# Performance work log

Hardware: AMD Instinct MI355X
Metric: run time of the kernel (lower is better)

The kernel has to match this reference:

```python
import jax, jax.numpy as jnp
import numpy as np
import math

B, S, H = 8, 4096, 1024
E, I, K = 8, 2048, 2
CAP_FACTOR = 1.0


def setup_inputs() -> dict:
    key = jax.random.key(0)
    k1, k2, k3, k4 = jax.random.split(key, 4)
    # kaiming_uniform (linear): bound = sqrt(3 / fan_in), fan_in = last dim
    def kaiming(k, shape):
        bound = math.sqrt(3.0 / shape[-1])
        return jax.random.uniform(k, shape, jnp.float32, -bound, bound)
    x = jax.random.normal(k1, (B, S, H), jnp.float32)
    expert_embeddings = kaiming(k2, (E, H))
    first_linear = kaiming(k3, (E, I, H))
    second_linear = kaiming(k4, (E, H, I))
    return {"x": x, "expert_embeddings": expert_embeddings,
            "first_linear": first_linear, "second_linear": second_linear}


def _router(x, expert_embeddings):
    # dot: [B, S, E]
    dot = jnp.einsum('bsh,eh->bse', x, expert_embeddings)
    n = dot.shape[0] * dot.shape[1]
    dot2 = dot.reshape(n, E)
    vals, idx = jax.lax.top_k(dot2, K)                       # [N, K]
    rows = jnp.arange(n)[:, None]
    masked = jnp.full_like(dot2, -jnp.inf).at[rows, idx].set(vals)
    return jax.nn.softmax(masked, axis=-1)                   # [N, E]


def reference(x, expert_embeddings, first_linear, second_linear):
    batch, seq, hidden = x.shape
    n_tokens = batch * seq
    expert_capacity = math.ceil(n_tokens / E * CAP_FACTOR)

    weights = _router(x, expert_embeddings)                  # [N, E]
    ones = (weights > 0).astype(weights.dtype)               # tokens routed to expert
    # capacity mask: keep first expert_capacity tokens (in token order) per expert
    cap_ones = jnp.where(jnp.cumsum(ones, axis=0) <= expert_capacity, ones, 0.0)
    caw = weights * cap_ones                                 # [N, E]

    # topk over token dim per expert -> selected token slots
    vals, idx = jax.lax.top_k(caw.T, expert_capacity)        # [E, C]
    index = idx.reshape(-1)                                  # [E*C]

    x_flat = x.reshape(n_tokens, hidden)
    tokens = x_flat[index].reshape(E, expert_capacity, hidden)   # gather

    inter = jax.nn.relu(jnp.einsum('ech,eih->eci', tokens, first_linear))
    out = jnp.einsum('eci,ehi->ech', inter, second_linear)
    out = out * vals[:, :, None]                             # weight by router prob

    final = jnp.zeros((n_tokens, hidden), x.dtype).at[index].add(
        out.reshape(-1, hidden))                             # scatter-add combine
    return final.reshape(x.shape)
```

## Files before the change

### kernel.cpp

```cpp
#include <hip/hip_runtime.h>
#include <stdint.h>

#define N_TOK 32768
#define HID   1024
#define NE    8
#define NI    2048
#define CAP   4096

typedef short s16x8 __attribute__((ext_vector_type(8)));
typedef float f32x4 __attribute__((ext_vector_type(4)));

__device__ __forceinline__ unsigned short f2bf(float f) {
    unsigned int u = __builtin_bit_cast(unsigned int, f);
    u += 0x7fffu + ((u >> 16) & 1u);
    return (unsigned short)(u >> 16);
}

__device__ __forceinline__ void gload16(const void* g, void* l) {
    __builtin_amdgcn_global_load_lds(
        (const __attribute__((address_space(1))) unsigned int*)(uintptr_t)g,
        (__attribute__((address_space(3))) unsigned int*)(unsigned int)(uintptr_t)l,
        16, 0, 0);
}

#define WAIT_LGKM0 asm volatile("s_waitcnt lgkmcnt(0)" ::: "memory")
#define WAIT_VM6   asm volatile("s_waitcnt vmcnt(6)" ::: "memory")
#define WAIT_VM0   asm volatile("s_waitcnt vmcnt(0)" ::: "memory")
#define SFENCE     __builtin_amdgcn_sched_barrier(0)
#define BARR       __builtin_amdgcn_s_barrier()

#define STAGE(Ms, rM, tile, h) do { \
    unsigned short* _d = Ms + (((tile) & 1) * 16384) + (h) * 8192 + wave * 1024; \
    gload16(rM[h][0] + (tile) * 64 + gsl8, _d); \
    gload16(rM[h][1] + (tile) * 64 + gsl8, _d + 512); } while (0)

#define MFMA16(AF, BF, NP) do { \
    __builtin_amdgcn_s_setprio(1); \
    _Pragma("unroll") \
    for (int mi = 0; mi < 8; ++mi) { \
        acc[mi][(NP)*2]   = __builtin_amdgcn_mfma_f32_16x16x32_bf16(AF[mi], BF[(NP)*2],   acc[mi][(NP)*2],   0, 0, 0); \
        acc[mi][(NP)*2+1] = __builtin_amdgcn_mfma_f32_16x16x32_bf16(AF[mi], BF[(NP)*2+1], acc[mi][(NP)*2+1], 0, 0, 0); \
    } \
    __builtin_amdgcn_s_setprio(0); \
} while (0)

__global__ __launch_bounds__(256) void cvt_kernel(
    const float* __restrict__ src, unsigned short* __restrict__ dst, size_t n8)
{
    size_t i = (size_t)blockIdx.x * 256 + threadIdx.x;
    size_t stride = (size_t)gridDim.x * 256;
    for (; i < n8; i += stride) {
        float4 a0 = ((const float4*)src)[2 * i];
        float4 a1 = ((const float4*)src)[2 * i + 1];
        uint4 p;
        p.x = f2bf(a0.x) | ((unsigned)f2bf(a0.y) << 16);
        p.y = f2bf(a0.z) | ((unsigned)f2bf(a0.w) << 16);
        p.z = f2bf(a1.x) | ((unsigned)f2bf(a1.y) << 16);
        p.w = f2bf(a1.z) | ((unsigned)f2bf(a1.w) << 16);
        ((uint4*)dst)[i] = p;
    }
}

__global__ __launch_bounds__(256) void router_kernel(
    const float* __restrict__ x, const float* __restrict__ emb,
    int2* __restrict__ r_e, float2* __restrict__ r_w,
    unsigned short* __restrict__ xb)
{
    int token = blockIdx.x * 4 + (threadIdx.x >> 6);
    int lane  = threadIdx.x & 63;
    const float4* xr = (const float4*)(x + (size_t)token * HID);
    const float4* er = (const float4*)emb;

    float a[NE];
#pragma unroll
    for (int e = 0; e < NE; ++e) a[e] = 0.f;
    uint2 pk[4];
#pragma unroll
    for (int j = 0; j < 4; ++j) {
        float4 v = xr[j * 64 + lane];
        pk[j].x = f2bf(v.x) | ((unsigned)f2bf(v.y) << 16);
        pk[j].y = f2bf(v.z) | ((unsigned)f2bf(v.w) << 16);
#pragma unroll
        for (int e = 0; e < NE; ++e) {
            float4 w = er[e * 256 + j * 64 + lane];
            a[e] += v.x * w.x + v.y * w.y + v.z * w.z + v.w * w.w;
        }
    }
    uint2* xbr = (uint2*)(xb + (size_t)token * HID);
#pragma unroll
    for (int j = 0; j < 4; ++j) xbr[j * 64 + lane] = pk[j];

#pragma unroll
    for (int e = 0; e < NE; ++e) {
        for (int off = 32; off; off >>= 1) a[e] += __shfl_xor(a[e], off);
    }
    if (lane == 0) {
        float v1 = -1e30f, v2 = -1e30f; int i1 = 0, i2 = 0;
#pragma unroll
        for (int e = 0; e < NE; ++e) {
            float v = a[e];
            if (v > v1) { v2 = v1; i2 = i1; v1 = v; i1 = e; }
            else if (v > v2) { v2 = v; i2 = e; }
        }
        float ex = __expf(v2 - v1);
        r_e[token] = make_int2(i1, i2);
        r_w[token] = make_float2(1.f / (1.f + ex), ex / (1.f + ex));
    }
}

__global__ __launch_bounds__(1024) void count_kernel(
    const int2* __restrict__ r_e, int* __restrict__ bc)
{
    __shared__ int cnt[NE];
    if (threadIdx.x < NE) cnt[threadIdx.x] = 0;
    __syncthreads();
    int n = blockIdx.x * 1024 + threadIdx.x;
    int2 e = r_e[n];
    atomicAdd(&cnt[e.x], 1);
    atomicAdd(&cnt[e.y], 1);
    __syncthreads();
    if (threadIdx.x < NE) bc[blockIdx.x * NE + threadIdx.x] = cnt[threadIdx.x];
}

__global__ void prefix_kernel(const int* __restrict__ bc, int* __restrict__ bb)
{
    int e = threadIdx.x;
    if (e >= NE) return;
    int run = 0;
    for (int b = 0; b < N_TOK / 1024; ++b) {
        bb[b * NE + e] = run;
        run += bc[b * NE + e];
    }
}

__global__ __launch_bounds__(1024) void assign_kernel(
    const int2* __restrict__ r_e, const float2* __restrict__ r_w,
    const int* __restrict__ bb,
    int* __restrict__ tok_list, float* __restrict__ w_list)
{
    __shared__ int wavecnt[16][NE];
    __shared__ int waveoff[16][NE];
    int tid = threadIdx.x, lane = tid & 63, wv = tid >> 6;
    int n = blockIdx.x * 1024 + tid;
    int2 e = r_e[n];
    float2 w = r_w[n];
    unsigned long long below = (1ull << lane) - 1ull;
    int rank0 = 0, rank1 = 0;
#pragma unroll
    for (int ex = 0; ex < NE; ++ex) {
        unsigned long long m = __ballot(e.x == ex || e.y == ex);
        if (lane == 0) wavecnt[wv][ex] = __popcll(m);
        int r = __popcll(m & below);
        if (e.x == ex) rank0 = r;
        if (e.y == ex) rank1 = r;
    }
    __syncthreads();
    if (tid < NE) {
        int run = 0;
        for (int w2 = 0; w2 < 16; ++w2) { waveoff[w2][tid] = run; run += wavecnt[w2][tid]; }
    }
    __syncthreads();
    int s0 = bb[blockIdx.x * NE + e.x] + waveoff[wv][e.x] + rank0;
    int s1 = bb[blockIdx.x * NE + e.y] + waveoff[wv][e.y] + rank1;
    if (s0 < CAP) { tok_list[e.x * CAP + s0] = n; w_list[e.x * CAP + s0] = w.x; }
    if (s1 < CAP) { tok_list[e.y * CAP + s1] = n; w_list[e.y * CAP + s1] = w.y; }
}

__global__ __launch_bounds__(512, 2) void gemm1_k(
    const unsigned short* __restrict__ xb,
    const unsigned short* __restrict__ w1b,
    const int* __restrict__ tok_list,
    unsigned short* __restrict__ inter,
    int eb)
{
    constexpr int K = HID, T = K / 64, NTN = NI / 256;
    __shared__ __align__(16) unsigned short smem[65536];
    unsigned short* As = smem;
    unsigned short* Bs = smem + 32768;

    const int nblk = gridDim.x;
    const int lin  = blockIdx.x;
    const int wg   = (lin & 7) * (nblk >> 3) + (lin >> 3);
    const int tn = wg % NTN;
    const int tm = (wg / NTN) & 15;
    const int ez = wg / (NTN * 16);
    const int e  = eb + ez;

    const int tid = threadIdx.x, lane = tid & 63, wave = tid >> 6;
    const int wr = wave >> 2, wc = wave & 3;
    const int gsl8 = ((lane & 7) ^ (lane >> 3)) * 8;
    const int aoff = (wr * 128 + (lane & 15)) * 64;
    const int boff = (wc * 64 + (lane & 15)) * 64;
    const int ph0 = ((lane >> 4) ^ (lane & 7)) * 8;
    const int ph1 = ((4 + (lane >> 4)) ^ (lane & 7)) * 8;
    const int rbase = wave * 16 + (lane >> 3);

    const int* tl = tok_list + e * CAP + tm * 256;
    const unsigned short* rA[2][2];
    const unsigned short* rB[2][2];
#pragma unroll
    for (int h = 0; h < 2; ++h)
#pragma unroll
        for (int j = 0; j < 2; ++j) {
            rA[h][j] = xb + (size_t)tl[h * 128 + rbase + j * 8] * K;
            rB[h][j] = w1b + ((size_t)e * NI + tn * 256 + h * 128 + rbase + j * 8) * K;
        }

    f32x4 acc[8][4];
#pragma unroll
    for (int i = 0; i < 8; ++i)
#pragma unroll
        for (int j = 0; j < 4; ++j) acc[i][j] = (f32x4)0.f;

    s16x8 afr[8], bfr0[4], bfr1[4];

    STAGE(As, rA, 0, 0); STAGE(As, rA, 0, 1);
    STAGE(Bs, rB, 0, 0); STAGE(Bs, rB, 0, 1);
    STAGE(Bs, rB, 1, 0); STAGE(Bs, rB, 1, 1);
    STAGE(As, rA, 1, 0);
    WAIT_VM6; SFENCE; BARR; SFENCE;

#pragma unroll 2
    for (int t = 0; t < T; ++t) {
        const int buf = (t & 1) * 16384;
        if (t + 1 < T) STAGE(As, rA, t + 1, 1);
#pragma unroll
        for (int mi = 0; mi < 8; ++mi)
            afr[mi] = *(const s16x8*)(As + buf + aoff + mi * 1024 + ph0);
#pragma unroll
        for (int ni = 0; ni < 4; ++ni) {
            bfr0[ni] = *(const s16x8*)(Bs + buf + boff + ni * 1024 + ph0);
            bfr1[ni] = *(const s16x8*)(Bs + buf + boff + ni * 1024 + ph1);
        }
        WAIT_LGKM0; SFENCE; BARR; SFENCE;
        MFMA16(afr, bfr0, 0);
        if (t + 2 < T) STAGE(Bs, rB, t + 2, 0);
        BARR; SFENCE;
        MFMA16(afr, bfr0, 1);
        if (t + 2 < T) STAGE(Bs, rB, t + 2, 1);
#pragma unroll
        for (int mi = 0; mi < 8; ++mi)
            afr[mi] = *(const s16x8*)(As + buf + aoff + mi * 1024 + ph1);
        WAIT_LGKM0; SFENCE; BARR; SFENCE;
        MFMA16(afr, bfr1, 0);
        if (t + 2 < T) STAGE(As, rA, t + 2, 0);
        if (t < T - 2) { WAIT_VM6; } else { WAIT_VM0; }
        SFENCE; BARR; SFENCE;
        MFMA16(afr, bfr1, 1);
    }

#pragma unroll
    for (int mi = 0; mi < 8; ++mi)
#pragma unroll
        for (int ni = 0; ni < 4; ++ni)
#pragma unroll
            for (int r = 0; r < 4; ++r) {
                int row = wr * 128 + mi * 16 + (lane >> 4) * 4 + r;
                int c   = wc * 64 + ni * 16 + (lane & 15);
                float v = acc[mi][ni][r];
                v = v > 0.f ? v : 0.f;
                smem[row * 256 + (((c >> 3) ^ (row & 7)) << 3) + (c & 7)] = f2bf(v);
            }
    __syncthreads();
    unsigned short* Cp = inter + ((size_t)ez * CAP + tm * 256) * NI + tn * 256;
#pragma unroll
    for (int it = 0; it < 16; ++it) {
        int v = tid + it * 512;
        int row = v >> 5, s = v & 31;
        uint4 val = *(const uint4*)&smem[row * 256 + ((s ^ (row & 7)) << 3)];
        *(uint4*)&Cp[(size_t)row * NI + s * 8] = val;
    }
}

__global__ __launch_bounds__(512, 2) void gemm2_k(
    const unsigned short* __restrict__ inter,
    const unsigned short* __restrict__ w2b,
    const int* __restrict__ tok_list,
    const float* __restrict__ w_list,
    float* __restrict__ out,
    int eb)
{
    constexpr int K = NI, T = K / 64, NTN = HID / 256;
    __shared__ __align__(16) unsigned short smem[65536];
    unsigned short* As = smem;
    unsigned short* Bs = smem + 32768;

    const int nblk = gridDim.x;
    const int lin  = blockIdx.x;
    const int wg   = (lin & 7) * (nblk >> 3) + (lin >> 3);
    const int tn = wg % NTN;
    const int tm = (wg / NTN) & 15;
    const int ez = wg / (NTN * 16);
    const int e  = eb + ez;

    const int tid = threadIdx.x, lane = tid & 63, wave = tid >> 6;
    const int wr = wave >> 2, wc = wave & 3;
    const int gsl8 = ((lane & 7) ^ (lane >> 3)) * 8;
    const int aoff = (wr * 128 + (lane & 15)) * 64;
    const int boff = (wc * 64 + (lane & 15)) * 64;
    const int ph0 = ((lane >> 4) ^ (lane & 7)) * 8;
    const int ph1 = ((4 + (lane >> 4)) ^ (lane & 7)) * 8;
    const int rbase = wave * 16 + (lane >> 3);

    const unsigned short* rA[2][2];
    const unsigned short* rB[2][2];
#pragma unroll
    for (int h = 0; h < 2; ++h)
#pragma unroll
        for (int j = 0; j < 2; ++j) {
            rA[h][j] = inter + ((size_t)ez * CAP + tm * 256 + h * 128 + rbase + j * 8) * (size_t)K;
            rB[h][j] = w2b + ((size_t)e * HID + tn * 256 + h * 128 + rbase + j * 8) * (size_t)K;
        }

    f32x4 acc[8][4];
#pragma unroll
    for (int i = 0; i < 8; ++i)
#pragma unroll
        for (int j = 0; j < 4; ++j) acc[i][j] = (f32x4)0.f;

    s16x8 afr[8], bfr0[4], bfr1[4];

    STAGE(As, rA, 0, 0); STAGE(As, rA, 0, 1);
    STAGE(Bs, rB, 0, 0); STAGE(Bs, rB, 0, 1);
    STAGE(Bs, rB, 1, 0); STAGE(Bs, rB, 1, 1);
    STAGE(As, rA, 1, 0);
    WAIT_VM6; SFENCE; BARR; SFENCE;

#pragma unroll 2
    for (int t = 0; t < T; ++t) {
        const int buf = (t & 1) * 16384;
        if (t + 1 < T) STAGE(As, rA, t + 1, 1);
#pragma unroll
        for (int mi = 0; mi < 8; ++mi)
            afr[mi] = *(const s16x8*)(As + buf + aoff + mi * 1024 + ph0);
#pragma unroll
        for (int ni = 0; ni < 4; ++ni) {
            bfr0[ni] = *(const s16x8*)(Bs + buf + boff + ni * 1024 + ph0);
            bfr1[ni] = *(const s16x8*)(Bs + buf + boff + ni * 1024 + ph1);
        }
        WAIT_LGKM0; SFENCE; BARR; SFENCE;
        MFMA16(afr, bfr0, 0);
        if (t + 2 < T) STAGE(Bs, rB, t + 2, 0);
        BARR; SFENCE;
        MFMA16(afr, bfr0, 1);
        if (t + 2 < T) STAGE(Bs, rB, t + 2, 1);
#pragma unroll
        for (int mi = 0; mi < 8; ++mi)
            afr[mi] = *(const s16x8*)(As + buf + aoff + mi * 1024 + ph1);
        WAIT_LGKM0; SFENCE; BARR; SFENCE;
        MFMA16(afr, bfr1, 0);
        if (t + 2 < T) STAGE(As, rA, t + 2, 0);
        if (t < T - 2) { WAIT_VM6; } else { WAIT_VM0; }
        SFENCE; BARR; SFENCE;
        MFMA16(afr, bfr1, 1);
    }

    const int* tl   = tok_list + e * CAP + tm * 256;
    const float* wl = w_list  + e * CAP + tm * 256;
#pragma unroll
    for (int mi = 0; mi < 8; ++mi)
#pragma unroll
        for (int r = 0; r < 4; ++r) {
            int rrow = wr * 128 + mi * 16 + (lane >> 4) * 4 + r;
            int tok  = tl[rrow];
            float w  = wl[rrow];
            float* orow = out + (size_t)tok * HID + tn * 256 + wc * 64;
#pragma unroll
            for (int ni = 0; ni < 4; ++ni)
                atomicAdd(&orow[ni * 16 + (lane & 15)], acc[mi][ni][r] * w);
        }
}

extern "C" void kernel_launch(void* const* d_in, const int* in_sizes, int n_in,
                              void* d_out, int out_size, void* d_ws, size_t ws_size,
                              hipStream_t stream)
{
    const float* x   = (const float*)d_in[0];
    const float* emb = (const float*)d_in[1];
    const float* W1  = (const float*)d_in[2];
    const float* W2  = (const float*)d_in[3];
    float* out = (float*)d_out;

    size_t off = 0;
    auto alloc = [&](size_t bytes) -> void* {
        void* p = (char*)d_ws + off;
        off += (bytes + 255) & ~(size_t)255;
        return p;
    };
    const size_t sz_w  = (size_t)NE * NI * HID * 2;
    const size_t sz_xb = (size_t)N_TOK * HID * 2;

    int*   tok_list = (int*)alloc((size_t)NE * CAP * 4);
    float* w_list   = (float*)alloc((size_t)NE * CAP * 4);
    unsigned short* w1b = (unsigned short*)alloc(sz_w);
    unsigned short* w2b = (unsigned short*)alloc(sz_w);
    unsigned short* xb  = (unsigned short*)alloc(sz_xb);

    unsigned short* inter = (unsigned short*)((char*)d_ws + off);
    size_t avail = ws_size > off ? ws_size - off : 0;
    const size_t per_e = (size_t)CAP * NI * 2;
    int G = (avail >= 8 * per_e) ? 8 : (avail >= 4 * per_e) ? 4
          : (avail >= 2 * per_e) ? 2 : 1;

    int2*   r_e = (int2*)inter;
    float2* r_w = (float2*)((char*)inter + (size_t)N_TOK * 8);
    int*    bc  = (int*)((char*)inter + (size_t)N_TOK * 16);
    int*    bb  = bc + (N_TOK / 1024) * NE;

    hipMemsetAsync(d_out, 0, (size_t)N_TOK * HID * 4, stream);
    hipMemsetAsync(tok_list, 0, (size_t)NE * CAP * 4, stream);
    hipMemsetAsync(w_list, 0, (size_t)NE * CAP * 4, stream);

    cvt_kernel<<<2048, 256, 0, stream>>>(W1, w1b, (size_t)NE * NI * HID / 8);
    cvt_kernel<<<2048, 256, 0, stream>>>(W2, w2b, (size_t)NE * HID * NI / 8);
    router_kernel<<<N_TOK / 4, 256, 0, stream>>>(x, emb, r_e, r_w, xb);
    count_kernel<<<N_TOK / 1024, 1024, 0, stream>>>(r_e, bc);
    prefix_kernel<<<1, 64, 0, stream>>>(bc, bb);
    assign_kernel<<<N_TOK / 1024, 1024, 0, stream>>>(r_e, r_w, bb, tok_list, w_list);

    for (int eb = 0; eb < NE; eb += G) {
        gemm1_k<<<dim3((NI / 256) * 16 * G), 512, 0, stream>>>(xb, w1b, tok_list, inter, eb);
        gemm2_k<<<dim3((HID / 256) * 16 * G), 512, 0, stream>>>(inter, w2b, tok_list, w_list, out, eb);
    }
}
```

Before: 471.4 us.

## Reshape GEMM wave tiling to 4x2 and interleave LDS reads with MFMA clusters

Changes the per-wave tile in both expert GEMMs from 128x64 to 64x128 (4x2 wave grid), splitting fragment loads into A/B halves. LDS reads are now interleaved with 4x4 MFMA clusters, and all next-tile global stages are issued in one group, cutting one barrier per k-step. This aims to overlap LDS latency with MFMA work and reduce synchronization. A __syncthreads is added before the epilogue because the LDS staging buffer is reused there.

After: 472.9 us. No clear change (+0.3%).

```diff
diff --git a/kernel.cpp b/kernel.cpp
--- a/kernel.cpp
+++ b/kernel.cpp
@@ -34,14 +34,27 @@
     gload16(rM[h][0] + (tile) * 64 + gsl8, _d); \
     gload16(rM[h][1] + (tile) * 64 + gsl8, _d + 512); } while (0)
 
-#define MFMA16(AF, BF, NP) do { \
+#define MFMA_CL(AF, BF, NB) do { \
     __builtin_amdgcn_s_setprio(1); \
     _Pragma("unroll") \
-    for (int mi = 0; mi < 8; ++mi) { \
-        acc[mi][(NP)*2]   = __builtin_amdgcn_mfma_f32_16x16x32_bf16(AF[mi], BF[(NP)*2],   acc[mi][(NP)*2],   0, 0, 0); \
-        acc[mi][(NP)*2+1] = __builtin_amdgcn_mfma_f32_16x16x32_bf16(AF[mi], BF[(NP)*2+1], acc[mi][(NP)*2+1], 0, 0, 0); \
-    } \
+    for (int mi = 0; mi < 4; ++mi) \
+    _Pragma("unroll") \
+    for (int nj = 0; nj < 4; ++nj) \
+        acc[mi][(NB) + nj] = __builtin_amdgcn_mfma_f32_16x16x32_bf16( \
+            AF[mi], BF[(NB) + nj], acc[mi][(NB) + nj], 0, 0, 0); \
     __builtin_amdgcn_s_setprio(0); \
+} while (0)
+
+#define RD_A(DST, PH) do { \
+    _Pragma("unroll") \
+    for (int mi = 0; mi < 4; ++mi) \
+        DST[mi] = *(const s16x8*)(As + buf + abase + mi * 1024 + (PH)); \
+} while (0)
+
+#define RD_B(DST, PH, NB) do { \
+    _Pragma("unroll") \
+    for (int nj = 0; nj < 4; ++nj) \
+        DST[(NB) + nj] = *(const s16x8*)(Bs + buf + bbase + ((NB) + nj) * 1024 + (PH)); \
 } while (0)
 
 __global__ __launch_bounds__(256) void cvt_kernel(
@@ -173,7 +186,7 @@
     unsigned short* __restrict__ inter,
     int eb)
 {
-    constexpr int K = HID, T = K / 64, NTN = NI / 256;
+    constexpr int K = HID, T = K / 64;
     __shared__ __align__(16) unsigned short smem[65536];
     unsigned short* As = smem;
     unsigned short* Bs = smem + 32768;
@@ -181,16 +194,16 @@
     const int nblk = gridDim.x;
     const int lin  = blockIdx.x;
     const int wg   = (lin & 7) * (nblk >> 3) + (lin >> 3);
-    const int tn = wg % NTN;
-    const int tm = (wg / NTN) & 15;
-    const int ez = wg / (NTN * 16);
+    const int tn = wg & 7;
+    const int tm = (wg >> 3) & 15;
+    const int ez = wg >> 7;
     const int e  = eb + ez;
 
     const int tid = threadIdx.x, lane = tid & 63, wave = tid >> 6;
-    const int wr = wave >> 2, wc = wave & 3;
+    const int wr = wave >> 1, wc = wave & 1;
     const int gsl8 = ((lane & 7) ^ (lane >> 3)) * 8;
-    const int aoff = (wr * 128 + (lane & 15)) * 64;
-    const int boff = (wc * 64 + (lane & 15)) * 64;
+    const int abase = (wr >> 1) * 8192 + (((wr & 1) * 64 + (lane & 15))) * 64;
+    const int bbase = wc * 8192 + (lane & 15) * 64;
     const int ph0 = ((lane >> 4) ^ (lane & 7)) * 8;
     const int ph1 = ((4 + (lane >> 4)) ^ (lane & 7)) * 8;
     const int rbase = wave * 16 + (lane >> 3);
@@ -206,57 +219,49 @@
             rB[h][j] = w1b + ((size_t)e * NI + tn * 256 + h * 128 + rbase + j * 8) * K;
         }
 
-    f32x4 acc[8][4];
-#pragma unroll
-    for (int i = 0; i < 8; ++i)
-#pragma unroll
-        for (int j = 0; j < 4; ++j) acc[i][j] = (f32x4)0.f;
-
-    s16x8 afr[8], bfr0[4], bfr1[4];
+    f32x4 acc[4][8];
+#pragma unroll
+    for (int i = 0; i < 4; ++i)
+#pragma unroll
+        for (int j = 0; j < 8; ++j) acc[i][j] = (f32x4)0.f;
+
+    s16x8 afr0[4], afr1[4], bfr0[8], bfr1[8];
 
     STAGE(As, rA, 0, 0); STAGE(As, rA, 0, 1);
     STAGE(Bs, rB, 0, 0); STAGE(Bs, rB, 0, 1);
+    STAGE(As, rA, 1, 0);
     STAGE(Bs, rB, 1, 0); STAGE(Bs, rB, 1, 1);
-    STAGE(As, rA, 1, 0);
     WAIT_VM6; SFENCE; BARR; SFENCE;
 
 #pragma unroll 2
     for (int t = 0; t < T; ++t) {
         const int buf = (t & 1) * 16384;
         if (t + 1 < T) STAGE(As, rA, t + 1, 1);
-#pragma unroll
-        for (int mi = 0; mi < 8; ++mi)
-            afr[mi] = *(const s16x8*)(As + buf + aoff + mi * 1024 + ph0);
-#pragma unroll
-        for (int ni = 0; ni < 4; ++ni) {
-            bfr0[ni] = *(const s16x8*)(Bs + buf + boff + ni * 1024 + ph0);
-            bfr1[ni] = *(const s16x8*)(Bs + buf + boff + ni * 1024 + ph1);
-        }
+        RD_A(afr0, ph0);
+        RD_B(bfr0, ph0, 0);
+        RD_B(bfr0, ph0, 4);
+        MFMA_CL(afr0, bfr0, 0);
+        RD_A(afr1, ph1);
+        MFMA_CL(afr0, bfr0, 4);
+        RD_B(bfr1, ph1, 0);
+        RD_B(bfr1, ph1, 4);
+        MFMA_CL(afr1, bfr1, 0);
         WAIT_LGKM0; SFENCE; BARR; SFENCE;
-        MFMA16(afr, bfr0, 0);
-        if (t + 2 < T) STAGE(Bs, rB, t + 2, 0);
-        BARR; SFENCE;
-        MFMA16(afr, bfr0, 1);
-        if (t + 2 < T) STAGE(Bs, rB, t + 2, 1);
-#pragma unroll
-        for (int mi = 0; mi < 8; ++mi)
-            afr[mi] = *(const s16x8*)(As + buf + aoff + mi * 1024 + ph1);
-        WAIT_LGKM0; SFENCE; BARR; SFENCE;
-        MFMA16(afr, bfr1, 0);
-        if (t + 2 < T) STAGE(As, rA, t + 2, 0);
+        if (t + 2 < T) { STAGE(As, rA, t + 2, 0); STAGE(Bs, rB, t + 2, 0); STAGE(Bs, rB, t + 2, 1); }
+        MFMA_CL(afr1, bfr1, 4);
         if (t < T - 2) { WAIT_VM6; } else { WAIT_VM0; }
         SFENCE; BARR; SFENCE;
-        MFMA16(afr, bfr1, 1);
-    }
-
-#pragma unroll
-    for (int mi = 0; mi < 8; ++mi)
-#pragma unroll
-        for (int ni = 0; ni < 4; ++ni)
+    }
+
+    __syncthreads();
+#pragma unroll
+    for (int mi = 0; mi < 4; ++mi)
+#pragma unroll
+        for (int ni = 0; ni < 8; ++ni)
 #pragma unroll
             for (int r = 0; r < 4; ++r) {
-                int row = wr * 128 + mi * 16 + (lane >> 4) * 4 + r;
-                int c   = wc * 64 + ni * 16 + (lane & 15);
+                int row = wr * 64 + mi * 16 + (lane >> 4) * 4 + r;
+                int c   = wc * 128 + ni * 16 + (lane & 15);
                 float v = acc[mi][ni][r];
                 v = v > 0.f ? v : 0.f;
                 smem[row * 256 + (((c >> 3) ^ (row & 7)) << 3) + (c & 7)] = f2bf(v);
@@ -280,7 +285,7 @@
     float* __restrict__ out,
     int eb)
 {
-    constexpr int K = NI, T = K / 64, NTN = HID / 256;
+    constexpr int K = NI, T = K / 64;
     __shared__ __align__(16) unsigned short smem[65536];
     unsigned short* As = smem;
     unsigned short* Bs = smem + 32768;
@@ -288,16 +293,16 @@
     const int nblk = gridDim.x;
     const int lin  = blockIdx.x;
     const int wg   = (lin & 7) * (nblk >> 3) + (lin >> 3);
-    const int tn = wg % NTN;
-    const int tm = (wg / NTN) & 15;
-    const int ez = wg / (NTN * 16);
+    const int tn = wg & 3;
+    const int tm = (wg >> 2) & 15;
+    const int ez = wg >> 6;
     const int e  = eb + ez;
 
     const int tid = threadIdx.x, lane = tid & 63, wave = tid >> 6;
-    const int wr = wave >> 2, wc = wave & 3;
+    const int wr = wave >> 1, wc = wave & 1;
     const int gsl8 = ((lane & 7) ^ (lane >> 3)) * 8;
-    const int aoff = (wr * 128 + (lane & 15)) * 64;
-    const int boff = (wc * 64 + (lane & 15)) * 64;
+    const int abase = (wr >> 1) * 8192 + (((wr & 1) * 64 + (lane & 15))) * 64;
+    const int bbase = wc * 8192 + (lane & 15) * 64;
     const int ph0 = ((lane >> 4) ^ (lane & 7)) * 8;
     const int ph1 = ((4 + (lane >> 4)) ^ (lane & 7)) * 8;
     const int rbase = wave * 16 + (lane >> 3);
@@ -312,61 +317,52 @@
             rB[h][j] = w2b + ((size_t)e * HID + tn * 256 + h * 128 + rbase + j * 8) * (size_t)K;
         }
 
-    f32x4 acc[8][4];
-#pragma unroll
-    for (int i = 0; i < 8; ++i)
-#pragma unroll
-        for (int j = 0; j < 4; ++j) acc[i][j] = (f32x4)0.f;
-
-    s16x8 afr[8], bfr0[4], bfr1[4];
+    f32x4 acc[4][8];
+#pragma unroll
+    for (int i = 0; i < 4; ++i)
+#pragma unroll
+        for (int j = 0; j < 8; ++j) acc[i][j] = (f32x4)0.f;
+
+    s16x8 afr0[4], afr1[4], bfr0[8], bfr1[8];
 
     STAGE(As, rA, 0, 0); STAGE(As, rA, 0, 1);
     STAGE(Bs, rB, 0, 0); STAGE(Bs, rB, 0, 1);
+    STAGE(As, rA, 1, 0);
     STAGE(Bs, rB, 1, 0); STAGE(Bs, rB, 1, 1);
-    STAGE(As, rA, 1, 0);
     WAIT_VM6; SFENCE; BARR; SFENCE;
 
 #pragma unroll 2
     for (int t = 0; t < T; ++t) {
         const int buf = (t & 1) * 16384;
         if (t + 1 < T) STAGE(As, rA, t + 1, 1);
-#pragma unroll
-        for (int mi = 0; mi < 8; ++mi)
-            afr[mi] = *(const s16x8*)(As + buf + aoff + mi * 1024 + ph0);
-#pragma unroll
-        for (int ni = 0; ni < 4; ++ni) {
-            bfr0[ni] = *(const s16x8*)(Bs + buf + boff + ni * 1024 + ph0);
-            bfr1[ni] = *(const s16x8*)(Bs + buf + boff + ni * 1024 + ph1);
-        }
+        RD_A(afr0, ph0);
+        RD_B(bfr0, ph0, 0);
+        RD_B(bfr0, ph0, 4);
+        MFMA_CL(afr0, bfr0, 0);
+        RD_A(afr1, ph1);
+        MFMA_CL(afr0, bfr0, 4);
+        RD_B(bfr1, ph1, 0);
+        RD_B(bfr1, ph1, 4);
+        MFMA_CL(afr1, bfr1, 0);
         WAIT_LGKM0; SFENCE; BARR; SFENCE;
-        MFMA16(afr, bfr0, 0);
-        if (t + 2 < T) STAGE(Bs, rB, t + 2, 0);
-        BARR; SFENCE;
-        MFMA16(afr, bfr0, 1);
-        if (t + 2 < T) STAGE(Bs, rB, t + 2, 1);
-#pragma unroll
-        for (int mi = 0; mi < 8; ++mi)
-            afr[mi] = *(const s16x8*)(As + buf + aoff + mi * 1024 + ph1);
-        WAIT_LGKM0; SFENCE; BARR; SFENCE;
-        MFMA16(afr, bfr1, 0);
-        if (t + 2 < T) STAGE(As, rA, t + 2, 0);
+        if (t + 2 < T) { STAGE(As, rA, t + 2, 0); STAGE(Bs, rB, t + 2, 0); STAGE(Bs, rB, t + 2, 1); }
+        MFMA_CL(afr1, bfr1, 4);
         if (t < T - 2) { WAIT_VM6; } else { WAIT_VM0; }
         SFENCE; BARR; SFENCE;
-        MFMA16(afr, bfr1, 1);
     }
 
     const int* tl   = tok_list + e * CAP + tm * 256;
     const float* wl = w_list  + e * CAP + tm * 256;
 #pragma unroll
-    for (int mi = 0; mi < 8; ++mi)
+    for (int mi = 0; mi < 4; ++mi)
 #pragma unroll
         for (int r = 0; r < 4; ++r) {
-            int rrow = wr * 128 + mi * 16 + (lane >> 4) * 4 + r;
+            int rrow = wr * 64 + mi * 16 + (lane >> 4) * 4 + r;
             int tok  = tl[rrow];
             float w  = wl[rrow];
-            float* orow = out + (size_t)tok * HID + tn * 256 + wc * 64;
-#pragma unroll
-            for (int ni = 0; ni < 4; ++ni)
+            float* orow = out + (size_t)tok * HID + tn * 256 + wc * 128;
+#pragma unroll
+            for (int ni = 0; ni < 8; ++ni)
                 atomicAdd(&orow[ni * 16 + (lane & 15)], acc[mi][ni][r] * w);
         }
 }
@@ -419,7 +415,7 @@
     assign_kernel<<<N_TOK / 1024, 1024, 0, stream>>>(r_e, r_w, bb, tok_list, w_list);
 
     for (int eb = 0; eb < NE; eb += G) {
-        gemm1_k<<<dim3((NI / 256) * 16 * G), 512, 0, stream>>>(xb, w1b, tok_list, inter, eb);
-        gemm2_k<<<dim3((HID / 256) * 16 * G), 512, 0, stream>>>(inter, w2b, tok_list, w_list, out, eb);
-    }
-}
+        gemm1_k<<<dim3(8 * 16 * G), 512, 0, stream>>>(xb, w1b, tok_list, inter, eb);
+        gemm2_k<<<dim3(4 * 16 * G), 512, 0, stream>>>(inter, w2b, tok_list, w_list, out, eb);
+    }
+}
```

## Restructure GEMM main loop into 8-phase quadrant pipeline with split A/B buffers

Applied to the files above, without the earlier changes.

Replaces the two-phase-per-tile GEMM K-loop in both expert GEMMs with an eight-phase schedule over two K-tiles. Each phase computes one 4x2 quadrant of the accumulator tile, and global-to-LDS loads are interleaved at finer granularity across separate A/B double buffers. The intent is to shrink register fragments per phase and overlap LDS reads and global loads more evenly with MFMA work. In exchange it adds many more barriers per tile and a different vmcnt wait depth, which could add synchronisation stalls.

Result: no change. 478.9 us (+1.6%).

```diff
diff --git a/kernel.cpp b/kernel.cpp
--- a/kernel.cpp
+++ b/kernel.cpp
@@ -24,25 +24,86 @@
 }
 
 #define WAIT_LGKM0 asm volatile("s_waitcnt lgkmcnt(0)" ::: "memory")
-#define WAIT_VM6   asm volatile("s_waitcnt vmcnt(6)" ::: "memory")
+#define WAIT_VM4   asm volatile("s_waitcnt vmcnt(4)" ::: "memory")
 #define WAIT_VM0   asm volatile("s_waitcnt vmcnt(0)" ::: "memory")
 #define SFENCE     __builtin_amdgcn_sched_barrier(0)
 #define BARR       __builtin_amdgcn_s_barrier()
 
-#define STAGE(Ms, rM, tile, h) do { \
-    unsigned short* _d = Ms + (((tile) & 1) * 16384) + (h) * 8192 + wave * 1024; \
-    gload16(rM[h][0] + (tile) * 64 + gsl8, _d); \
-    gload16(rM[h][1] + (tile) * 64 + gsl8, _d + 512); } while (0)
-
-#define MFMA16(AF, BF, NP) do { \
+#define STG(DST, SRC, H, TT) do { \
+    unsigned short* _d = (DST) + (H) * 8192 + wave * 1024; \
+    gload16(SRC[H][0] + (size_t)(TT) * 64 + gsl8, _d); \
+    gload16(SRC[H][1] + (size_t)(TT) * 64 + gsl8, _d + 512); } while (0)
+
+#define RD_A(BASE, MH) do { \
+    _Pragma("unroll") for (int m2 = 0; m2 < 4; ++m2) \
+    _Pragma("unroll") for (int ks = 0; ks < 2; ++ks) \
+        afr[m2*2+ks] = *(const s16x8*)((BASE) + aoff + (MH)*4096 + m2*1024 + phs[ks]); } while (0)
+
+#define RD_B(BF, BASE, NH) do { \
+    _Pragma("unroll") for (int n2 = 0; n2 < 2; ++n2) \
+    _Pragma("unroll") for (int ks = 0; ks < 2; ++ks) \
+        BF[n2*2+ks] = *(const s16x8*)((BASE) + boff + (NH)*2048 + n2*1024 + phs[ks]); } while (0)
+
+#define MFMA_Q(MH, NH, BF) do { \
     __builtin_amdgcn_s_setprio(1); \
-    _Pragma("unroll") \
-    for (int mi = 0; mi < 8; ++mi) { \
-        acc[mi][(NP)*2]   = __builtin_amdgcn_mfma_f32_16x16x32_bf16(AF[mi], BF[(NP)*2],   acc[mi][(NP)*2],   0, 0, 0); \
-        acc[mi][(NP)*2+1] = __builtin_amdgcn_mfma_f32_16x16x32_bf16(AF[mi], BF[(NP)*2+1], acc[mi][(NP)*2+1], 0, 0, 0); \
-    } \
-    __builtin_amdgcn_s_setprio(0); \
-} while (0)
+    _Pragma("unroll") for (int m2 = 0; m2 < 4; ++m2) \
+    _Pragma("unroll") for (int n2 = 0; n2 < 2; ++n2) \
+    _Pragma("unroll") for (int ks = 0; ks < 2; ++ks) \
+        acc[(MH)*4+m2][(NH)*2+n2] = __builtin_amdgcn_mfma_f32_16x16x32_bf16( \
+            afr[m2*2+ks], BF[n2*2+ks], acc[(MH)*4+m2][(NH)*2+n2], 0, 0, 0); \
+    __builtin_amdgcn_s_setprio(0); } while (0)
+
+#define KLOOP8(T) \
+    for (int it = 0; it < (T) / 2; ++it) { \
+        const int t0 = 2 * it, t1 = t0 + 1; \
+        const bool lastI = (it == (T) / 2 - 1); \
+         \
+        STG(Abuf1, rA, 1, t1); \
+        RD_A(Abuf0, 0); RD_B(bfr0, Bbuf0, 0); \
+        SFENCE; BARR; WAIT_LGKM0; SFENCE; \
+        MFMA_Q(0, 0, bfr0); BARR; SFENCE; \
+         \
+        STG(Bbuf1, rB, 1, t1); \
+        RD_B(bfr1, Bbuf0, 1); \
+        SFENCE; BARR; WAIT_LGKM0; SFENCE; \
+        MFMA_Q(0, 1, bfr1); BARR; SFENCE; \
+         \
+        if (t0 + 2 < (T)) STG(Bbuf0, rB, 0, t0 + 2); \
+        RD_A(Abuf0, 1); \
+        SFENCE; BARR; WAIT_LGKM0; SFENCE; \
+        MFMA_Q(1, 0, bfr0); BARR; SFENCE; \
+         \
+        if (t0 + 2 < (T)) STG(Bbuf0, rB, 1, t0 + 2); \
+        if (lastI) { WAIT_VM0; } else { WAIT_VM4; } \
+        SFENCE; BARR; SFENCE; \
+        MFMA_Q(1, 1, bfr1); BARR; SFENCE; \
+         \
+        if (t0 + 2 < (T)) STG(Abuf0, rA, 0, t0 + 2); \
+        RD_A(Abuf1, 0); RD_B(bfr0, Bbuf1, 0); \
+        SFENCE; BARR; WAIT_LGKM0; SFENCE; \
+        MFMA_Q(0, 0, bfr0); BARR; SFENCE; \
+         \
+        if (t0 + 2 < (T)) STG(Abuf0, rA, 1, t0 + 2); \
+        RD_B(bfr1, Bbuf1, 1); \
+        SFENCE; BARR; WAIT_LGKM0; SFENCE; \
+        MFMA_Q(0, 1, bfr1); BARR; SFENCE; \
+         \
+        if (t1 + 2 < (T)) STG(Bbuf1, rB, 0, t1 + 2); \
+        RD_A(Abuf1, 1); \
+        SFENCE; BARR; WAIT_LGKM0; SFENCE; \
+        MFMA_Q(1, 0, bfr0); BARR; SFENCE; \
+         \
+        if (t1 + 2 < (T)) STG(Abuf1, rA, 0, t1 + 2); \
+        if (lastI) { WAIT_VM0; } else { WAIT_VM4; } \
+        SFENCE; BARR; SFENCE; \
+        MFMA_Q(1, 1, bfr1); BARR; SFENCE; \
+    }
+
+#define KPROLOGUE \
+    STG(Abuf0, rA, 0, 0); STG(Abuf0, rA, 1, 0); \
+    STG(Bbuf0, rB, 0, 0); STG(Bbuf0, rB, 1, 0); \
+    STG(Bbuf1, rB, 0, 1); STG(Abuf1, rA, 0, 1); \
+    WAIT_VM4; SFENCE; BARR; SFENCE;
 
 __global__ __launch_bounds__(256) void cvt_kernel(
     const float* __restrict__ src, unsigned short* __restrict__ dst, size_t n8)
@@ -166,6 +227,7 @@
     if (s1 < CAP) { tok_list[e.y * CAP + s1] = n; w_list[e.y * CAP + s1] = w.y; }
 }
 
+
 __global__ __launch_bounds__(512, 2) void gemm1_k(
     const unsigned short* __restrict__ xb,
     const unsigned short* __restrict__ w1b,
@@ -173,27 +235,28 @@
     unsigned short* __restrict__ inter,
     int eb)
 {
-    constexpr int K = HID, T = K / 64, NTN = NI / 256;
+    constexpr int K = HID, T = K / 64;
     __shared__ __align__(16) unsigned short smem[65536];
-    unsigned short* As = smem;
-    unsigned short* Bs = smem + 32768;
+    unsigned short* const Abuf0 = smem;
+    unsigned short* const Bbuf0 = smem + 16384;
+    unsigned short* const Abuf1 = smem + 32768;
+    unsigned short* const Bbuf1 = smem + 49152;
 
     const int nblk = gridDim.x;
     const int lin  = blockIdx.x;
     const int wg   = (lin & 7) * (nblk >> 3) + (lin >> 3);
-    const int tn = wg % NTN;
-    const int tm = (wg / NTN) & 15;
-    const int ez = wg / (NTN * 16);
+    const int tn = wg & 7;
+    const int tm = (wg >> 3) & 15;
+    const int ez = wg >> 7;
     const int e  = eb + ez;
 
     const int tid = threadIdx.x, lane = tid & 63, wave = tid >> 6;
     const int wr = wave >> 2, wc = wave & 3;
-    const int gsl8 = ((lane & 7) ^ (lane >> 3)) * 8;
+    const int gsl8 = ((lane & 7) ^ ((lane >> 3) & 7)) * 8;
     const int aoff = (wr * 128 + (lane & 15)) * 64;
     const int boff = (wc * 64 + (lane & 15)) * 64;
-    const int ph0 = ((lane >> 4) ^ (lane & 7)) * 8;
-    const int ph1 = ((4 + (lane >> 4)) ^ (lane & 7)) * 8;
-    const int rbase = wave * 16 + (lane >> 3);
+    const int phs[2] = { (((lane >> 4)) ^ (lane & 7)) * 8,
+                         ((4 + (lane >> 4)) ^ (lane & 7)) * 8 };
 
     const int* tl = tok_list + e * CAP + tm * 256;
     const unsigned short* rA[2][2];
@@ -202,8 +265,9 @@
     for (int h = 0; h < 2; ++h)
 #pragma unroll
         for (int j = 0; j < 2; ++j) {
-            rA[h][j] = xb + (size_t)tl[h * 128 + rbase + j * 8] * K;
-            rB[h][j] = w1b + ((size_t)e * NI + tn * 256 + h * 128 + rbase + j * 8) * K;
+            int row = h * 128 + wave * 16 + (lane >> 3) + j * 8;
+            rA[h][j] = xb + (size_t)tl[row] * K;
+            rB[h][j] = w1b + ((size_t)e * NI + tn * 256 + row) * K;
         }
 
     f32x4 acc[8][4];
@@ -214,41 +278,11 @@
 
     s16x8 afr[8], bfr0[4], bfr1[4];
 
-    STAGE(As, rA, 0, 0); STAGE(As, rA, 0, 1);
-    STAGE(Bs, rB, 0, 0); STAGE(Bs, rB, 0, 1);
-    STAGE(Bs, rB, 1, 0); STAGE(Bs, rB, 1, 1);
-    STAGE(As, rA, 1, 0);
-    WAIT_VM6; SFENCE; BARR; SFENCE;
-
-#pragma unroll 2
-    for (int t = 0; t < T; ++t) {
-        const int buf = (t & 1) * 16384;
-        if (t + 1 < T) STAGE(As, rA, t + 1, 1);
-#pragma unroll
-        for (int mi = 0; mi < 8; ++mi)
-            afr[mi] = *(const s16x8*)(As + buf + aoff + mi * 1024 + ph0);
-#pragma unroll
-        for (int ni = 0; ni < 4; ++ni) {
-            bfr0[ni] = *(const s16x8*)(Bs + buf + boff + ni * 1024 + ph0);
-            bfr1[ni] = *(const s16x8*)(Bs + buf + boff + ni * 1024 + ph1);
-        }
-        WAIT_LGKM0; SFENCE; BARR; SFENCE;
-        MFMA16(afr, bfr0, 0);
-        if (t + 2 < T) STAGE(Bs, rB, t + 2, 0);
-        BARR; SFENCE;
-        MFMA16(afr, bfr0, 1);
-        if (t + 2 < T) STAGE(Bs, rB, t + 2, 1);
-#pragma unroll
-        for (int mi = 0; mi < 8; ++mi)
-            afr[mi] = *(const s16x8*)(As + buf + aoff + mi * 1024 + ph1);
-        WAIT_LGKM0; SFENCE; BARR; SFENCE;
-        MFMA16(afr, bfr1, 0);
-        if (t + 2 < T) STAGE(As, rA, t + 2, 0);
-        if (t < T - 2) { WAIT_VM6; } else { WAIT_VM0; }
-        SFENCE; BARR; SFENCE;
-        MFMA16(afr, bfr1, 1);
-    }
-
+    KPROLOGUE
+#pragma unroll 1
+    KLOOP8(T)
+
+    __syncthreads();
 #pragma unroll
     for (int mi = 0; mi < 8; ++mi)
 #pragma unroll
@@ -264,8 +298,8 @@
     __syncthreads();
     unsigned short* Cp = inter + ((size_t)ez * CAP + tm * 256) * NI + tn * 256;
 #pragma unroll
-    for (int it = 0; it < 16; ++it) {
-        int v = tid + it * 512;
+    for (int itv = 0; itv < 16; ++itv) {
+        int v = tid + itv * 512;
         int row = v >> 5, s = v & 31;
         uint4 val = *(const uint4*)&smem[row * 256 + ((s ^ (row & 7)) << 3)];
         *(uint4*)&Cp[(size_t)row * NI + s * 8] = val;
@@ -280,27 +314,28 @@
     float* __restrict__ out,
     int eb)
 {
-    constexpr int K = NI, T = K / 64, NTN = HID / 256;
+    constexpr int K = NI, T = K / 64;
     __shared__ __align__(16) unsigned short smem[65536];
-    unsigned short* As = smem;
-    unsigned short* Bs = smem + 32768;
+    unsigned short* const Abuf0 = smem;
+    unsigned short* const Bbuf0 = smem + 16384;
+    unsigned short* const Abuf1 = smem + 32768;
+    unsigned short* const Bbuf1 = smem + 49152;
 
     const int nblk = gridDim.x;
     const int lin  = blockIdx.x;
     const int wg   = (lin & 7) * (nblk >> 3) + (lin >> 3);
-    const int tn = wg % NTN;
-    const int tm = (wg / NTN) & 15;
-    const int ez = wg / (NTN * 16);
+    const int tn = wg & 3;
+    const int tm = (wg >> 2) & 15;
+    const int ez = wg >> 6;
     const int e  = eb + ez;
 
     const int tid = threadIdx.x, lane = tid & 63, wave = tid >> 6;
     const int wr = wave >> 2, wc = wave & 3;
-    const int gsl8 = ((lane & 7) ^ (lane >> 3)) * 8;
+    const int gsl8 = ((lane & 7) ^ ((lane >> 3) & 7)) * 8;
     const int aoff = (wr * 128 + (lane & 15)) * 64;
     const int boff = (wc * 64 + (lane & 15)) * 64;
-    const int ph0 = ((lane >> 4) ^ (lane & 7)) * 8;
-    const int ph1 = ((4 + (lane >> 4)) ^ (lane & 7)) * 8;
-    const int rbase = wave * 16 + (lane >> 3);
+    const int phs[2] = { (((lane >> 4)) ^ (lane & 7)) * 8,
+                         ((4 + (lane >> 4)) ^ (lane & 7)) * 8 };
 
     const unsigned short* rA[2][2];
     const unsigned short* rB[2][2];
@@ -308,8 +343,9 @@
     for (int h = 0; h < 2; ++h)
 #pragma unroll
         for (int j = 0; j < 2; ++j) {
-            rA[h][j] = inter + ((size_t)ez * CAP + tm * 256 + h * 128 + rbase + j * 8) * (size_t)K;
-            rB[h][j] = w2b + ((size_t)e * HID + tn * 256 + h * 128 + rbase + j * 8) * (size_t)K;
+            int row = h * 128 + wave * 16 + (lane >> 3) + j * 8;
+            rA[h][j] = inter + ((size_t)ez * CAP + tm * 256 + row) * (size_t)K;
+            rB[h][j] = w2b + ((size_t)e * HID + tn * 256 + row) * (size_t)K;
         }
 
     f32x4 acc[8][4];
@@ -320,40 +356,9 @@
 
     s16x8 afr[8], bfr0[4], bfr1[4];
 
-    STAGE(As, rA, 0, 0); STAGE(As, rA, 0, 1);
-    STAGE(Bs, rB, 0, 0); STAGE(Bs, rB, 0, 1);
-    STAGE(Bs, rB, 1, 0); STAGE(Bs, rB, 1, 1);
-    STAGE(As, rA, 1, 0);
-    WAIT_VM6; SFENCE; BARR; SFENCE;
-
-#pragma unroll 2
-    for (int t = 0; t < T; ++t) {
-        const int buf = (t & 1) * 16384;
-        if (t + 1 < T) STAGE(As, rA, t + 1, 1);
-#pragma unroll
-        for (int mi = 0; mi < 8; ++mi)
-            afr[mi] = *(const s16x8*)(As + buf + aoff + mi * 1024 + ph0);
-#pragma unroll
-        for (int ni = 0; ni < 4; ++ni) {
-            bfr0[ni] = *(const s16x8*)(Bs + buf + boff + ni * 1024 + ph0);
-            bfr1[ni] = *(const s16x8*)(Bs + buf + boff + ni * 1024 + ph1);
-        }
-        WAIT_LGKM0; SFENCE; BARR; SFENCE;
-        MFMA16(afr, bfr0, 0);
-        if (t + 2 < T) STAGE(Bs, rB, t + 2, 0);
-        BARR; SFENCE;
-        MFMA16(afr, bfr0, 1);
-        if (t + 2 < T) STAGE(Bs, rB, t + 2, 1);
-#pragma unroll
-        for (int mi = 0; mi < 8; ++mi)
-            afr[mi] = *(const s16x8*)(As + buf + aoff + mi * 1024 + ph1);
-        WAIT_LGKM0; SFENCE; BARR; SFENCE;
-        MFMA16(afr, bfr1, 0);
-        if (t + 2 < T) STAGE(As, rA, t + 2, 0);
-        if (t < T - 2) { WAIT_VM6; } else { WAIT_VM0; }
-        SFENCE; BARR; SFENCE;
-        MFMA16(afr, bfr1, 1);
-    }
+    KPROLOGUE
+#pragma unroll 1
+    KLOOP8(T)
 
     const int* tl   = tok_list + e * CAP + tm * 256;
     const float* wl = w_list  + e * CAP + tm * 256;
@@ -419,7 +424,7 @@
     assign_kernel<<<N_TOK / 1024, 1024, 0, stream>>>(r_e, r_w, bb, tok_list, w_list);
 
     for (int eb = 0; eb < NE; eb += G) {
-        gemm1_k<<<dim3((NI / 256) * 16 * G), 512, 0, stream>>>(xb, w1b, tok_list, inter, eb);
-        gemm2_k<<<dim3((HID / 256) * 16 * G), 512, 0, stream>>>(inter, w2b, tok_list, w_list, out, eb);
-    }
-}
+        gemm1_k<<<dim3(8 * 16 * G), 512, 0, stream>>>(xb, w1b, tok_list, inter, eb);
+        gemm2_k<<<dim3(4 * 16 * G), 512, 0, stream>>>(inter, w2b, tok_list, w_list, out, eb);
+    }
+}
```
